# Kernel tuning notes

Hardware: AMD Instinct MI355X
Metric: run time of the kernel (lower is better)

Reference implementation:

```python
import jax, jax.numpy as jnp
import numpy as np

D_MODEL = 2048
NUM_HEADS = 32
NUM_KV_HEADS = 8
HEAD_DIM = D_MODEL // NUM_HEADS  # 64
KV_GROUPS = NUM_HEADS // NUM_KV_HEADS  # 4


def setup_inputs() -> dict:
    key = jax.random.key(0)
    k1, k2, k3, k4, k5 = jax.random.split(key, 5)
    scale = 0.02
    h_bsd = jax.random.normal(k1, (2, 2048, D_MODEL), dtype=jnp.float32)
    # nn.Linear weights stored as [out_features, in_features]
    w_q = jax.random.normal(k2, (NUM_HEADS * HEAD_DIM, D_MODEL), dtype=jnp.float32) * scale
    w_k = jax.random.normal(k3, (NUM_KV_HEADS * HEAD_DIM, D_MODEL), dtype=jnp.float32) * scale
    w_v = jax.random.normal(k4, (NUM_KV_HEADS * HEAD_DIM, D_MODEL), dtype=jnp.float32) * scale
    w_o = jax.random.normal(k5, (D_MODEL, NUM_HEADS * HEAD_DIM), dtype=jnp.float32) * scale
    return {"h_bsd": h_bsd, "w_q": w_q, "w_k": w_k, "w_v": w_v, "w_o": w_o}


def reference(h_bsd, w_q, w_k, w_v, w_o):
    b, s, _ = h_bsd.shape
    # projections (Linear without bias: x @ W.T)
    q = (h_bsd @ w_q.T).reshape(b, s, NUM_HEADS, HEAD_DIM).transpose(0, 2, 1, 3)      # [b, nq, s, h]
    k = (h_bsd @ w_k.T).reshape(b, s, NUM_KV_HEADS, HEAD_DIM).transpose(0, 2, 1, 3)   # [b, nkv, l, h]
    v = (h_bsd @ w_v.T).reshape(b, s, NUM_KV_HEADS, HEAD_DIM).transpose(0, 2, 1, 3)   # [b, nkv, l, h]
    # repeat_interleave over head dim to expand kv heads to query heads
    k = jnp.repeat(k, KV_GROUPS, axis=1)  # [b, nq, l, h]
    v = jnp.repeat(v, KV_GROUPS, axis=1)
    attn = jnp.einsum('bqsh,bqlh->bqsl', q, k) / jnp.sqrt(jnp.float32(HEAD_DIM))
    attn = jax.nn.softmax(attn, axis=-1)
    out = jnp.einsum('bqsl,bqlh->bqsh', attn, v)            # [b, nq, s, h]
    out = out.transpose(0, 2, 1, 3).reshape(b, s, D_MODEL)  # [b, s, d]
    return out @ w_o.T
```

## Files before the change

kernel.cpp:

```cpp
#include <hip/hip_runtime.h>
#include <stdint.h>

typedef unsigned short ushort_t;
typedef __attribute__((ext_vector_type(8))) short short8;
typedef __attribute__((ext_vector_type(4))) float floatx4;


__device__ __forceinline__ ushort_t f2bf(float f) {
  unsigned int u = __builtin_bit_cast(unsigned int, f);
  u += 0x7fffu + ((u >> 16) & 1u);
  return (ushort_t)(u >> 16);
}

__device__ __forceinline__ void gld16(const void* g, void* l) {
  __builtin_amdgcn_global_load_lds(
      (__attribute__((address_space(1))) void*)(void*)(g),
      (__attribute__((address_space(3))) void*)(l), 16, 0, 0);
}


__global__ __launch_bounds__(256)
void cast_all_kernel(const float* __restrict__ h, const float* __restrict__ wq,
                     const float* __restrict__ wk, const float* __restrict__ wv,
                     const float* __restrict__ wo,
                     ushort_t* __restrict__ h_bf, ushort_t* __restrict__ wqkv_bf,
                     ushort_t* __restrict__ wo_bf, float qscale) {
  long i = (long)blockIdx.x * 256 + threadIdx.x;
  const float4* src; ushort4* dst; float sc = 1.0f;
  if (i < 2097152L)       { src = (const float4*)h  + i;             dst = (ushort4*)h_bf + i; }
  else if (i < 3145728L)  { src = (const float4*)wq + (i - 2097152); dst = (ushort4*)wqkv_bf + (i - 2097152); sc = qscale; }
  else if (i < 3407872L)  { src = (const float4*)wk + (i - 3145728); dst = (ushort4*)wqkv_bf + (i - 3145728) + 1048576; }
  else if (i < 3670016L)  { src = (const float4*)wv + (i - 3407872); dst = (ushort4*)wqkv_bf + (i - 3407872) + 1310720; }
  else                    { src = (const float4*)wo + (i - 3670016); dst = (ushort4*)wo_bf + (i - 3670016); }
  float4 v = *src; ushort4 o;
  o.x = f2bf(v.x * sc); o.y = f2bf(v.y * sc);
  o.z = f2bf(v.z * sc); o.w = f2bf(v.w * sc);
  *dst = o;
}


template <int OM>
__global__ __launch_bounds__(256)
void gemm_bt(const ushort_t* __restrict__ A, const ushort_t* __restrict__ B,
             void* __restrict__ Cp, int M, int N, int K) {
  __shared__ ushort_t As[128 * 32];
  __shared__ ushort_t Bs[128 * 32];
  const int tid  = threadIdx.x;
  const int wave = tid >> 6, lane = tid & 63;
  const int quad = lane >> 4, l16 = lane & 15;
  const int wm = (wave >> 1) * 64, wn = (wave & 1) * 64;
  const int bm = blockIdx.x * 128, bn = blockIdx.y * 128;
  const int srow = lane >> 2, scc = lane & 3;

  floatx4 acc[4][4] = {};

  for (int k0 = 0; k0 < K; k0 += 32) {
#pragma unroll
    for (int r = 0; r < 2; ++r) {
      int c   = wave * 2 + r;
      int row = c * 16 + srow;
      int g   = scc ^ ((row >> 1) & 3);
      gld16(A + (long)(bm + row) * K + k0 + g * 8, As + c * 512 + lane * 8);
      gld16(B + (long)(bn + row) * K + k0 + g * 8, Bs + c * 512 + lane * 8);
    }
    __syncthreads();

    short8 af[4], bf[4];
#pragma unroll
    for (int i = 0; i < 4; ++i) {
      int m = wm + i * 16 + l16;
      af[i] = *(const short8*)(As + m * 32 + ((quad ^ ((m >> 1) & 3)) * 8));
      int n = wn + i * 16 + l16;
      bf[i] = *(const short8*)(Bs + n * 32 + ((quad ^ ((n >> 1) & 3)) * 8));
    }
#pragma unroll
    for (int i = 0; i < 4; ++i)
#pragma unroll
      for (int j = 0; j < 4; ++j)
        acc[i][j] = __builtin_amdgcn_mfma_f32_16x16x32_bf16(af[i], bf[j], acc[i][j], 0, 0, 0);
    __syncthreads();
  }

#pragma unroll
  for (int i = 0; i < 4; ++i)
#pragma unroll
    for (int j = 0; j < 4; ++j)
#pragma unroll
      for (int r = 0; r < 4; ++r) {
        int row = bm + wm + i * 16 + quad * 4 + r;
        int col = bn + wn + j * 16 + l16;
        if (OM == 0) ((ushort_t*)Cp)[(long)row * N + col] = f2bf(acc[i][j][r]);
        else         ((float*)Cp)[(long)row * N + col]    = acc[i][j][r];
      }
}


__global__ __launch_bounds__(256)
void transpose_v(const ushort_t* __restrict__ QKV, ushort_t* __restrict__ Vtg) {
  __shared__ ushort_t t[64 * 72];
  const int tid = threadIdx.x;
  const int b = blockIdx.z, kvh = blockIdx.y, l0 = blockIdx.x * 64;
#pragma unroll
  for (int r = 0; r < 2; ++r) {
    int idx = tid + r * 256;
    int row = idx >> 3, sub = idx & 7;
    short8 v = *(const short8*)(QKV + (long)(b * 2048 + l0 + row) * 3072 + 2560 + kvh * 64 + sub * 8);
    *(short8*)(t + row * 72 + sub * 8) = v;
  }
  __syncthreads();
#pragma unroll
  for (int r = 0; r < 2; ++r) {
    int idx = tid + r * 256;
    int hd = idx >> 3, sub = idx & 7;
    short8 o;
#pragma unroll
    for (int e = 0; e < 8; ++e) o[e] = (short)t[(sub * 8 + e) * 72 + hd];
    *(short8*)(Vtg + (long)((b * 8 + kvh) * 64 + hd) * 2048 + l0 + sub * 8) = o;
  }
}


__global__ __launch_bounds__(256)
void attn_kernel(const ushort_t* __restrict__ QKV, const ushort_t* __restrict__ Vtg,
                 ushort_t* __restrict__ AO) {
  __shared__ ushort_t Ks[2][64 * 64];
  __shared__ ushort_t Vt[2][64 * 64];
  __shared__ ushort_t Pt[128 * 64];
  __shared__ float    sumb[128];

  const int tid  = threadIdx.x;
  const int wave = tid >> 6, lane = tid & 63;
  const int quad = lane >> 4, l16 = lane & 15;
  const int b = blockIdx.z, h = blockIdx.y;
  const int q0 = blockIdx.x * 128;
  const int kvh = h >> 2;
  const long tok0 = (long)b * 2048 + q0;

  short8 qf[2][2];
#pragma unroll
  for (int kb = 0; kb < 2; ++kb)
#pragma unroll
    for (int j = 0; j < 2; ++j)
      qf[kb][j] = *(const short8*)(QKV + (tok0 + wave * 32 + j * 16 + l16) * 3072
                                   + h * 64 + kb * 32 + quad * 8);

  floatx4 oacc[2][4] = {};
  float lsum[2] = {0.f, 0.f};

  const int lr = lane >> 3, sub = lane & 7;
  const int g = sub ^ lr;
  const ushort_t* Kbase = QKV + (long)b * 2048 * 3072 + 2048 + kvh * 64;
  const ushort_t* Vbase = Vtg + (long)(b * 8 + kvh) * 64 * 2048;

  auto stage = [&](int bf_, int l0) {
#pragma unroll
    for (int r = 0; r < 2; ++r) {
      int c = wave * 2 + r;
      int row = c * 8 + lr;
      gld16(Kbase + (long)(l0 + row) * 3072 + g * 8, Ks[bf_] + c * 512 + lane * 8);
      gld16(Vbase + (long)row * 2048 + l0 + g * 8, Vt[bf_] + c * 512 + lane * 8);
    }
  };

  stage(0, 0);

  for (int it = 0; it < 32; ++it) {
    __syncthreads();
    if (it + 1 < 32) stage((it + 1) & 1, (it + 1) * 64);
    const ushort_t* Kc = Ks[it & 1];
    const ushort_t* Vc = Vt[it & 1];

    floatx4 s[4][2] = {};
#pragma unroll
    for (int kb = 0; kb < 2; ++kb) {
      short8 kf[4];
#pragma unroll
      for (int i = 0; i < 4; ++i)
        kf[i] = *(const short8*)(Kc + (i * 16 + l16) * 64 + (((kb * 4 + quad) ^ (l16 & 7)) * 8));
#pragma unroll
      for (int i = 0; i < 4; ++i)
#pragma unroll
        for (int j = 0; j < 2; ++j)
          s[i][j] = __builtin_amdgcn_mfma_f32_16x16x32_bf16(kf[i], qf[kb][j], s[i][j], 0, 0, 0);
    }

#pragma unroll
    for (int i = 0; i < 4; ++i)
#pragma unroll
      for (int j = 0; j < 2; ++j) {
        float p0 = __builtin_amdgcn_exp2f(s[i][j][0]);
        float p1 = __builtin_amdgcn_exp2f(s[i][j][1]);
        float p2 = __builtin_amdgcn_exp2f(s[i][j][2]);
        float p3 = __builtin_amdgcn_exp2f(s[i][j][3]);
        lsum[j] += (p0 + p1) + (p2 + p3);
        uint2 w;
        w.x = __builtin_amdgcn_perm(__builtin_bit_cast(unsigned int, p1),
                                    __builtin_bit_cast(unsigned int, p0), 0x07060302u);
        w.y = __builtin_amdgcn_perm(__builtin_bit_cast(unsigned int, p3),
                                    __builtin_bit_cast(unsigned int, p2), 0x07060302u);
        int q = wave * 32 + j * 16 + l16;
        int idx = q * 64 + (((i * 2 + (quad >> 1)) ^ (l16 & 7)) * 8) + (quad & 1) * 4;
        *(uint2*)(Pt + idx) = w;
      }

#pragma unroll
    for (int kb = 0; kb < 2; ++kb) {
      short8 pf[2], vf[4];
#pragma unroll
      for (int im = 0; im < 2; ++im)
        pf[im] = *(const short8*)(Pt + (wave * 32 + im * 16 + l16) * 64
                                  + (((kb * 4 + quad) ^ (l16 & 7)) * 8));
#pragma unroll
      for (int n = 0; n < 4; ++n)
        vf[n] = *(const short8*)(Vc + (n * 16 + l16) * 64
                                 + (((kb * 4 + quad) ^ (l16 & 7)) * 8));
#pragma unroll
      for (int im = 0; im < 2; ++im)
#pragma unroll
        for (int n = 0; n < 4; ++n)
          oacc[im][n] = __builtin_amdgcn_mfma_f32_16x16x32_bf16(pf[im], vf[n], oacc[im][n], 0, 0, 0);
    }
  }

#pragma unroll
  for (int j = 0; j < 2; ++j) {
    float sv = lsum[j];
    sv += __shfl_xor(sv, 16);
    sv += __shfl_xor(sv, 32);
    if (quad == 0) sumb[wave * 32 + j * 16 + l16] = sv;
  }
  __syncthreads();

  float inv[2][4];
#pragma unroll
  for (int im = 0; im < 2; ++im)
#pragma unroll
    for (int r = 0; r < 4; ++r)
      inv[im][r] = 1.0f / sumb[wave * 32 + im * 16 + quad * 4 + r];

#pragma unroll
  for (int im = 0; im < 2; ++im)
#pragma unroll
    for (int n = 0; n < 4; ++n)
#pragma unroll
      for (int r = 0; r < 4; ++r) {
        long t = tok0 + wave * 32 + im * 16 + quad * 4 + r;
        AO[t * 2048 + h * 64 + n * 16 + l16] = f2bf(oacc[im][n][r] * inv[im][r]);
      }
}


extern "C" void kernel_launch(void* const* d_in, const int* in_sizes, int n_in,
                              void* d_out, int out_size, void* d_ws, size_t ws_size,
                              hipStream_t stream) {
  const float* h  = (const float*)d_in[0];
  const float* wq = (const float*)d_in[1];
  const float* wk = (const float*)d_in[2];
  const float* wv = (const float*)d_in[3];
  const float* wo = (const float*)d_in[4];
  float* out = (float*)d_out;

  const int BS = 4096, D = 2048, KV = 512, NQKV = 3072;

  ushort_t* h_bf    = (ushort_t*)d_ws;
  ushort_t* wqkv_bf = h_bf + (long)BS * D;
  ushort_t* wo_bf   = wqkv_bf + (long)NQKV * D;
  ushort_t* QKV     = wo_bf + (long)D * D;
  ushort_t* Vtg     = QKV + (long)BS * NQKV;
  ushort_t* AO      = h_bf;

  const float qscale = 0.125f * 1.44269504088896f;

  cast_all_kernel<<<4718592 / 256, 256, 0, stream>>>(h, wq, wk, wv, wo,
                                                     h_bf, wqkv_bf, wo_bf, qscale);

  gemm_bt<0><<<dim3(BS / 128, NQKV / 128), 256, 0, stream>>>(h_bf, wqkv_bf, QKV, BS, NQKV, D);

  transpose_v<<<dim3(32, 8, 2), 256, 0, stream>>>(QKV, Vtg);

  attn_kernel<<<dim3(2048 / 128, 32, 2), 256, 0, stream>>>(QKV, Vtg, AO);

  gemm_bt<1><<<dim3(BS / 128, D / 128), 256, 0, stream>>>(AO, wo_bf, out, BS, D, D);
}
```

Before: 332.5 us.

## Compute softmax row sums via MFMA with ones and halve P tile LDS

The attention kernel now computes the softmax denominator with an extra MFMA against a vector of bf16 ones, which removes the per-lane scalar sums, the shuffle reduction, the shared sum buffer and the final block barrier. The P tile is written and consumed in two half-width chunks interleaved with the PV MFMAs, halving its LDS footprint, and launch bounds request 4 blocks per CU. The aim is higher occupancy and less VALU work, paid for with extra MFMA issue. The denominator is now summed from the bf16-rounded P values, which changes rounding slightly.

```diff
diff --git a/kernel.cpp b/kernel.cpp
--- a/kernel.cpp
+++ b/kernel.cpp
@@ -120,13 +120,12 @@
 }
 
 
-__global__ __launch_bounds__(256)
+__global__ __launch_bounds__(256, 4)
 void attn_kernel(const ushort_t* __restrict__ QKV, const ushort_t* __restrict__ Vtg,
                  ushort_t* __restrict__ AO) {
   __shared__ ushort_t Ks[2][64 * 64];
   __shared__ ushort_t Vt[2][64 * 64];
-  __shared__ ushort_t Pt[128 * 64];
-  __shared__ float    sumb[128];
+  __shared__ ushort_t Pt[128 * 32];
 
   const int tid  = threadIdx.x;
   const int wave = tid >> 6, lane = tid & 63;
@@ -145,7 +144,11 @@
                                    + h * 64 + kb * 32 + quad * 8);
 
   floatx4 oacc[2][4] = {};
-  float lsum[2] = {0.f, 0.f};
+  floatx4 osum[2] = {};
+
+  short8 bones;
+#pragma unroll
+  for (int e = 0; e < 8; ++e) bones[e] = (short)0x3F80;
 
   const int lr = lane >> 3, sub = lane & 7;
   const int g = sub ^ lr;
@@ -185,68 +188,59 @@
     }
 
 #pragma unroll
-    for (int i = 0; i < 4; ++i)
-#pragma unroll
-      for (int j = 0; j < 2; ++j) {
-        float p0 = __builtin_amdgcn_exp2f(s[i][j][0]);
-        float p1 = __builtin_amdgcn_exp2f(s[i][j][1]);
-        float p2 = __builtin_amdgcn_exp2f(s[i][j][2]);
-        float p3 = __builtin_amdgcn_exp2f(s[i][j][3]);
-        lsum[j] += (p0 + p1) + (p2 + p3);
-        uint2 w;
-        w.x = __builtin_amdgcn_perm(__builtin_bit_cast(unsigned int, p1),
-                                    __builtin_bit_cast(unsigned int, p0), 0x07060302u);
-        w.y = __builtin_amdgcn_perm(__builtin_bit_cast(unsigned int, p3),
-                                    __builtin_bit_cast(unsigned int, p2), 0x07060302u);
-        int q = wave * 32 + j * 16 + l16;
-        int idx = q * 64 + (((i * 2 + (quad >> 1)) ^ (l16 & 7)) * 8) + (quad & 1) * 4;
-        *(uint2*)(Pt + idx) = w;
-      }
-
-#pragma unroll
-    for (int kb = 0; kb < 2; ++kb) {
+    for (int hh = 0; hh < 2; ++hh) {
+#pragma unroll
+      for (int ii = 0; ii < 2; ++ii) {
+        int i = hh * 2 + ii;
+#pragma unroll
+        for (int j = 0; j < 2; ++j) {
+          float p0 = __builtin_amdgcn_exp2f(s[i][j][0]);
+          float p1 = __builtin_amdgcn_exp2f(s[i][j][1]);
+          float p2 = __builtin_amdgcn_exp2f(s[i][j][2]);
+          float p3 = __builtin_amdgcn_exp2f(s[i][j][3]);
+          uint2 w;
+          w.x = __builtin_amdgcn_perm(__builtin_bit_cast(unsigned int, p1),
+                                      __builtin_bit_cast(unsigned int, p0), 0x07060302u);
+          w.y = __builtin_amdgcn_perm(__builtin_bit_cast(unsigned int, p3),
+                                      __builtin_bit_cast(unsigned int, p2), 0x07060302u);
+          int q = wave * 32 + j * 16 + l16;
+          int c = ii * 2 + (quad >> 1);
+          int idx = q * 32 + ((c ^ (l16 & 3)) * 8) + (quad & 1) * 4;
+          *(uint2*)(Pt + idx) = w;
+        }
+      }
       short8 pf[2], vf[4];
 #pragma unroll
       for (int im = 0; im < 2; ++im)
-        pf[im] = *(const short8*)(Pt + (wave * 32 + im * 16 + l16) * 64
-                                  + (((kb * 4 + quad) ^ (l16 & 7)) * 8));
+        pf[im] = *(const short8*)(Pt + (wave * 32 + im * 16 + l16) * 32
+                                  + ((quad ^ (l16 & 3)) * 8));
 #pragma unroll
       for (int n = 0; n < 4; ++n)
         vf[n] = *(const short8*)(Vc + (n * 16 + l16) * 64
-                                 + (((kb * 4 + quad) ^ (l16 & 7)) * 8));
-#pragma unroll
-      for (int im = 0; im < 2; ++im)
+                                 + (((hh * 4 + quad) ^ (l16 & 7)) * 8));
+#pragma unroll
+      for (int im = 0; im < 2; ++im) {
 #pragma unroll
         for (int n = 0; n < 4; ++n)
           oacc[im][n] = __builtin_amdgcn_mfma_f32_16x16x32_bf16(pf[im], vf[n], oacc[im][n], 0, 0, 0);
-    }
-  }
-
-#pragma unroll
-  for (int j = 0; j < 2; ++j) {
-    float sv = lsum[j];
-    sv += __shfl_xor(sv, 16);
-    sv += __shfl_xor(sv, 32);
-    if (quad == 0) sumb[wave * 32 + j * 16 + l16] = sv;
-  }
-  __syncthreads();
-
-  float inv[2][4];
-#pragma unroll
-  for (int im = 0; im < 2; ++im)
-#pragma unroll
-    for (int r = 0; r < 4; ++r)
-      inv[im][r] = 1.0f / sumb[wave * 32 + im * 16 + quad * 4 + r];
-
-#pragma unroll
-  for (int im = 0; im < 2; ++im)
+        osum[im] = __builtin_amdgcn_mfma_f32_16x16x32_bf16(pf[im], bones, osum[im], 0, 0, 0);
+      }
+    }
+  }
+
+#pragma unroll
+  for (int im = 0; im < 2; ++im) {
+    floatx4 inv;
+#pragma unroll
+    for (int r = 0; r < 4; ++r) inv[r] = 1.0f / osum[im][r];
 #pragma unroll
     for (int n = 0; n < 4; ++n)
 #pragma unroll
       for (int r = 0; r < 4; ++r) {
         long t = tok0 + wave * 32 + im * 16 + quad * 4 + r;
-        AO[t * 2048 + h * 64 + n * 16 + l16] = f2bf(oacc[im][n][r] * inv[im][r]);
-      }
+        AO[t * 2048 + h * 64 + n * 16 + l16] = f2bf(oacc[im][n][r] * inv[r]);
+      }
+  }
 }
 
 
```

Result: faster. 320.9 us (-3.5%).
